# Performance work log

Measured on AMD Instinct MI355X. Metric: run time of the kernel, lower is better.

## Reference

```python
import jax, jax.numpy as jnp
import numpy as np

N_WAY = 5
K_SHOT = 5
TEMPERATURE = 2.0
EPS = 1e-8


def setup_inputs() -> dict:
    key = jax.random.key(0)
    k1, k2, k3, k4 = jax.random.split(key, 4)
    b, q, c, h, w = 4, 75, 640, 10, 10
    support_xf = jax.random.normal(k1, (b, N_WAY * K_SHOT, c, h, w), jnp.float32)
    query_xf = jax.random.normal(k2, (b, q, c, h, w), jnp.float32)
    support_y = jax.random.randint(k3, (b, N_WAY * K_SHOT), 0, N_WAY)
    query_y = jax.random.randint(k4, (b, q), 0, N_WAY)
    return {"support_xf": support_xf, "support_y": support_y,
            "query_xf": query_xf, "query_y": query_y}


def reference(support_xf, support_y, query_xf, query_y):
    b, q, c, h, w = query_xf.shape
    M_q = h * w
    M_s = K_SHOT * h * w  # larger_shot == 'average' -> concat shot descriptors

    # support: [b, n_way*k_shot, c, h, w] -> [b, n_way, c, k_shot*h*w]
    sup = support_xf.reshape(b, N_WAY, K_SHOT, c, h * w)
    sup = jnp.transpose(sup, (0, 1, 3, 2, 4)).reshape(b, N_WAY, c, M_s)
    qf = query_xf.reshape(b, q, c, M_q)

    # cosine similarity over channel dim
    sn = sup / (jnp.linalg.norm(sup, axis=2, keepdims=True) + EPS)
    qn = qf / (jnp.linalg.norm(qf, axis=2, keepdims=True) + EPS)
    # S: [b, q, n_way, M_q, M_s]
    S = jnp.einsum('bqcm,bwcn->bqwmn', qn, sn)

    S_max = S.max(-1)  # [b, q, n_way, M_q]

    # nearest support descriptor (classes merged) for each query descriptor
    S_merged = jnp.transpose(S, (0, 1, 3, 2, 4)).reshape(b, q, M_q, N_WAY * M_s)
    query_nearest = jnp.argmax(S_merged, axis=-1)  # [b, q, M_q]

    # top-2 over class dim of per-class max similarity
    top2 = jax.lax.top_k(jnp.moveaxis(S_max, 2, -1), 2)[0]  # [b, q, M_q, 2]
    query_class_diff = top2[..., 0] - top2[..., 1]  # [b, q, M_q]

    # scatter diffs to the chosen support slot, take max over query positions
    diffs_m = jax.nn.one_hot(query_nearest, N_WAY * M_s, dtype=jnp.float32) \
        * query_class_diff[..., None]  # [b, q, M_q, n_way*M_s]
    diffs_max_nearest = jnp.argmax(diffs_m, axis=-2)  # [b, q, n_way*M_s]

    # mutual-nearest mask: query m is kept iff it is the best query for its slot
    sel = jnp.take_along_axis(diffs_max_nearest, query_nearest, axis=-1)  # [b,q,M_q]
    diff_mask = (sel == jnp.arange(M_q)).astype(jnp.float32) * TEMPERATURE

    predict = (S_max * diff_mask[:, :, None, :]).sum(-1).reshape(b * q, N_WAY)

    logp = jax.nn.log_softmax(predict, axis=-1)
    loss = -jnp.mean(jnp.take_along_axis(logp, query_y.reshape(-1, 1), axis=1))
    return loss
```

## Files before the change

kernel.cpp:

```cpp
#include <hip/hip_runtime.h>
#include <math.h>

#define BB 4
#define QQ 75
#define CC 640
#define HW 100
#define NWAY 5
#define KSHOT 5
#define MS 500
#define MSP 512
#define MTOT 7500
#define MPAD 7680
#define TEMPER 2.0f
#define EPSN 1e-8f
#define LB 32768
#define NCH 8

typedef _Float16 v8h __attribute__((ext_vector_type(8)));
typedef float v4f __attribute__((ext_vector_type(4)));

__device__ inline void splitv(const float* x, v8h& hi, v8h& lo) {
#pragma unroll
    for (int j = 0; j < 8; ++j) {
        _Float16 h = (_Float16)x[j];
        float r0 = x[j] - (float)h;
        hi[j] = h; lo[j] = (_Float16)r0;
    }
}

typedef __attribute__((address_space(3))) unsigned int lds_uint;
typedef __attribute__((address_space(1))) const unsigned int glb_uint;
__device__ inline void gl_lds16(const void* g, void* l) {
    __builtin_amdgcn_global_load_lds((glb_uint*)g, (lds_uint*)l, 16, 0, 0);
}

__global__ __launch_bounds__(128) void norms(const float* __restrict__ qx,
                                             const float* __restrict__ sup,
                                             float* __restrict__ invq,
                                             float* __restrict__ invs,
                                             float* __restrict__ out) {
    int bid = blockIdx.x, t = threadIdx.x;
    if (bid == 0 && t == 0) out[0] = 0.f;
    const float* src; float* dst;
    if (bid < BB * QQ) { src = qx + (size_t)bid * CC * HW; dst = invq + bid * HW; }
    else { int bs = bid - BB * QQ; src = sup + (size_t)bs * CC * HW; dst = invs + bs * HW; }
    if (t < HW) {
        float ss = 0.f;
        for (int c = 0; c < CC; ++c) { float v = src[c * HW + t]; ss += v * v; }
        dst[t] = 1.f / (sqrtf(ss) + EPSN);
    }
}

__global__ __launch_bounds__(256) void prep_AB(const float* __restrict__ qx,
                                               const float* __restrict__ sup,
                                               const float* __restrict__ invs,
                                               _Float16* __restrict__ Ahi,
                                               _Float16* __restrict__ Alo,
                                               _Float16* __restrict__ Bhi,
                                               _Float16* __restrict__ Blo) {
    int g = blockIdx.x;
    const float* src; const float* inv = 0;
    _Float16 *dh, *dl;
    int ct;
    if (g < BB * QQ * 10) {
        int bq = g / 10; ct = g % 10;
        int b = bq / QQ, qi = bq % QQ;
        src = qx + ((size_t)bq * CC + ct * 64) * HW;
        size_t rowbase = (size_t)b * MPAD + qi * HW;
        dh = Ahi + rowbase * CC; dl = Alo + rowbase * CC;
    } else {
        int h = g - BB * QQ * 10;
        int bs = h / 10; ct = h % 10;
        int b = bs / 25, s = bs % 25, w = s / KSHOT, shot = s % KSHOT;
        src = sup + ((size_t)bs * CC + ct * 64) * HW;
        size_t rowbase = (size_t)(b * NWAY + w) * MSP + shot * HW;
        dh = Bhi + rowbase * CC; dl = Blo + rowbase * CC;
        inv = invs + bs * HW;
    }
    __shared__ float tile[64 * 101];
    __shared__ float invt[HW];
    int t = threadIdx.x;
    if (t < HW) invt[t] = inv ? inv[t] : 1.f;
    for (int i = t; i < 64 * HW; i += 256) tile[(i / HW) * 101 + (i % HW)] = src[i];
    __syncthreads();
    for (int cell = t; cell < 800; cell += 256) {
        int p = cell >> 3, oct = cell & 7;
        float iv = invt[p];
        float x[8];
#pragma unroll
        for (int j = 0; j < 8; ++j) x[j] = tile[(oct * 8 + j) * 101 + p] * iv;
        v8h hi, lo; splitv(x, hi, lo);
        size_t off = (size_t)p * CC + ct * 64 + oct * 8;
        *(v8h*)(dh + off) = hi;
        *(v8h*)(dl + off) = lo;
    }
}

__global__ __launch_bounds__(256, 2) void simkernel(
        const _Float16* __restrict__ Ahi, const _Float16* __restrict__ Alo,
        const _Float16* __restrict__ Bhi, const _Float16* __restrict__ Blo,
        float* __restrict__ pmax, unsigned short* __restrict__ pidx) {
    __shared__ char lds_raw[2 * LB];

    int bid = blockIdx.x;
    int mt = bid % 60; int t2 = bid / 60;
    int nt = t2 % 20;  int b = t2 / 20;
    int m0 = mt * 128;
    int w = nt >> 2, n0w = (nt & 3) * 128;

    int tid = threadIdx.x;
    int lane = tid & 63;
    int wvu = __builtin_amdgcn_readfirstlane(tid >> 6);

    const char* abase[4];
    abase[0] = (const char*)(Ahi + ((size_t)b * MPAD + m0) * CC);
    abase[1] = (const char*)(Alo + ((size_t)b * MPAD + m0) * CC);
    abase[2] = (const char*)(Bhi + ((size_t)(b * NWAY + w) * MSP + n0w) * CC);
    abase[3] = (const char*)(Blo + ((size_t)(b * NWAY + w) * MSP + n0w) * CC);

    int rr0 = lane >> 2;
    int oct = (lane & 3) ^ ((lane >> 3) & 3);
    int laneoff = rr0 * (CC * 2) + oct * 16;

    const char* segsrc[8];
    int segoff[8];
#pragma unroll
    for (int s = 0; s < 8; ++s) {
        int g = wvu * 8 + s;
        segsrc[s] = abase[g >> 3] + (size_t)((g & 7) * 16) * (CC * 2) + laneoff;
        segoff[s] = g * 1024;
    }

    int wv = tid >> 6;
    int mrow_w = (wv >> 1) * 64;
    int ncol_w = (wv & 1) * 64;
    int lq = lane >> 4, lc = lane & 15;

    int idxA[4], idxB[4];
#pragma unroll
    for (int mf = 0; mf < 4; ++mf) {
        int row = mrow_w + mf * 16 + lc;
        idxA[mf] = row * 4 + (lq ^ ((row >> 1) & 3));
    }
#pragma unroll
    for (int nf = 0; nf < 4; ++nf) {
        int row = ncol_w + nf * 16 + lc;
        idxB[nf] = row * 4 + (lq ^ ((row >> 1) & 3));
    }

    v4f acc[4][4];
#pragma unroll
    for (int mf = 0; mf < 4; ++mf)
#pragma unroll
        for (int nf = 0; nf < 4; ++nf) acc[mf][nf] = (v4f)0.f;

#pragma unroll
    for (int s = 0; s < 8; ++s)
        gl_lds16(segsrc[s], lds_raw + segoff[s]);

    for (int ch = 0; ch < 20; ++ch) {
        __syncthreads();
        if (ch < 19) {
            int choff = (ch + 1) * 64;
            int dbase = ((ch + 1) & 1) * LB;
#pragma unroll
            for (int s = 0; s < 8; ++s)
                gl_lds16(segsrc[s] + choff, lds_raw + dbase + segoff[s]);
        }
        char* cbuf = lds_raw + (ch & 1) * LB;
        v8h* AHI = (v8h*)cbuf;
        v8h* ALO = (v8h*)(cbuf + 8192);
        v8h* BHI = (v8h*)(cbuf + 16384);
        v8h* BLO = (v8h*)(cbuf + 24576);

        v8h ahi[4], alo[4];
#pragma unroll
        for (int mf = 0; mf < 4; ++mf) { ahi[mf] = AHI[idxA[mf]]; alo[mf] = ALO[idxA[mf]]; }
#pragma unroll
        for (int nf = 0; nf < 4; ++nf) {
            v8h bhi = BHI[idxB[nf]], blo = BLO[idxB[nf]];
#pragma unroll
            for (int mf = 0; mf < 4; ++mf) {
                acc[mf][nf] = __builtin_amdgcn_mfma_f32_16x16x32_f16(ahi[mf], bhi, acc[mf][nf], 0, 0, 0);
                acc[mf][nf] = __builtin_amdgcn_mfma_f32_16x16x32_f16(ahi[mf], blo, acc[mf][nf], 0, 0, 0);
                acc[mf][nf] = __builtin_amdgcn_mfma_f32_16x16x32_f16(alo[mf], bhi, acc[mf][nf], 0, 0, 0);
            }
        }
    }

    int chunk = (nt & 3) * 2 + (wv & 1);
#pragma unroll
    for (int mf = 0; mf < 4; ++mf) {
#pragma unroll
        for (int r = 0; r < 4; ++r) {
            float v = -__builtin_inff(); int idx = 0x7fffffff;
#pragma unroll
            for (int nf = 0; nf < 4; ++nf) {
                int n_way = n0w + ncol_w + nf * 16 + lc;
                float cv = acc[mf][nf][r];
                if (n_way < MS && cv > v) { v = cv; idx = n_way; }
            }
#pragma unroll
            for (int msk = 1; msk < 16; msk <<= 1) {
                float ov = __shfl_xor(v, msk);
                int oi = __shfl_xor(idx, msk);
                if (ov > v || (ov == v && oi < idx)) { v = ov; idx = oi; }
            }
            if (lc == 0) {
                int mrow = m0 + mrow_w + mf * 16 + lq * 4 + r;
                size_t o = ((size_t)(b * NWAY + w) * NCH + chunk) * MPAD + mrow;
                pmax[o] = v;
                pidx[o] = (unsigned short)(idx & 0xffff);
            }
        }
    }
}

__global__ void norm_support(const float* __restrict__ sup, float* __restrict__ snre) {
    int bid = blockIdx.x;
    int b = bid / 25, s = bid % 25;
    int w = s / KSHOT, shot = s % KSHOT;
    const float* src = sup + (size_t)bid * CC * HW;
    float* dst = snre + ((size_t)(b * NWAY + w)) * CC * MSP + shot * HW;
    __shared__ float inv[HW];
    int t = threadIdx.x;
    if (t < HW) {
        float ss = 0.f;
        for (int c = 0; c < CC; ++c) { float v = src[c * HW + t]; ss += v * v; }
        inv[t] = 1.f / (sqrtf(ss) + EPSN);
    }
    __syncthreads();
    for (int i = t; i < CC * HW; i += 256) {
        int c = i / HW, p = i % HW;
        dst[c * MSP + p] = src[i] * inv[p];
    }
    if (shot == KSHOT - 1) {
        float* padbase = snre + ((size_t)(b * NWAY + w)) * CC * MSP;
        for (int i = t; i < CC * (MSP - MS); i += 256) {
            int c = i / (MSP - MS), j = i % (MSP - MS);
            padbase[c * MSP + MS + j] = 0.f;
        }
    }
}

__global__ __launch_bounds__(256) void simkernel_fb(
        const float* __restrict__ qx, const float* __restrict__ snre,
        float* __restrict__ pmax, unsigned short* __restrict__ pidx) {
    __shared__ char lds_fb[49152];
    v8h* AHI = (v8h*)(lds_fb);
    v8h* ALO = (v8h*)(lds_fb + 8192);
    v8h* BHI = (v8h*)(lds_fb + 16384);
    v8h* BLO = (v8h*)(lds_fb + 32768);

    int bid = blockIdx.x;
    int mt = bid % 60; int t2 = bid / 60;
    int nt = t2 % 10;  int b = t2 / 10;
    int m0 = mt * 128;
    int w = nt >> 1;
    int n0w = (nt & 1) * 256;

    int tid = threadIdx.x;
    const float* Abase = qx + (size_t)b * QQ * CC * HW;
    const float* Bbase = snre + (size_t)(b * NWAY + w) * CC * MSP;

    int oct = tid & 3;
    int arow = tid >> 2;
    int aqi[2], ap[2];
#pragma unroll
    for (int pass = 0; pass < 2; ++pass) {
        int mg = m0 + arow + pass * 64;
        if (mg >= MTOT) mg = 0;
        aqi[pass] = mg / HW; ap[pass] = mg % HW;
    }

    v4f acc[4][8];
#pragma unroll
    for (int mf = 0; mf < 4; ++mf)
#pragma unroll
        for (int nf = 0; nf < 8; ++nf) acc[mf][nf] = (v4f)0.f;

    int lane = tid & 63;
    int wv = tid >> 6;
    int mrow_w = (wv >> 1) * 64;
    int ncol_w = (wv & 1) * 128;
    int lq = lane >> 4, lc = lane & 15;

    for (int ch = 0; ch < 20; ++ch) {
        int c0 = ch * 32 + oct * 8;
        __syncthreads();
#pragma unroll
        for (int pass = 0; pass < 2; ++pass) {
            const float* src = Abase + ((size_t)aqi[pass] * CC + c0) * HW + ap[pass];
            float x[8];
#pragma unroll
            for (int j = 0; j < 8; ++j) x[j] = src[j * HW];
            v8h hi, lo; splitv(x, hi, lo);
            int cell = (arow + pass * 64) * 4 + oct;
            AHI[cell] = hi; ALO[cell] = lo;
        }
#pragma unroll
        for (int pass = 0; pass < 4; ++pass) {
            int nrow = arow + pass * 64;
            const float* src = Bbase + (size_t)c0 * MSP + n0w + nrow;
            float x[8];
#pragma unroll
            for (int j = 0; j < 8; ++j) x[j] = src[j * MSP];
            v8h hi, lo; splitv(x, hi, lo);
            int cell = nrow * 4 + oct;
            BHI[cell] = hi; BLO[cell] = lo;
        }
        __syncthreads();

        v8h ahi[4], alo[4];
#pragma unroll
        for (int mf = 0; mf < 4; ++mf) {
            int idx = (mrow_w + mf * 16 + lc) * 4 + lq;
            ahi[mf] = AHI[idx]; alo[mf] = ALO[idx];
        }
#pragma unroll
        for (int nf = 0; nf < 8; ++nf) {
            int idx = (ncol_w + nf * 16 + lc) * 4 + lq;
            v8h bhi = BHI[idx], blo = BLO[idx];
#pragma unroll
            for (int mf = 0; mf < 4; ++mf) {
                acc[mf][nf] = __builtin_amdgcn_mfma_f32_16x16x32_f16(ahi[mf], bhi, acc[mf][nf], 0, 0, 0);
                acc[mf][nf] = __builtin_amdgcn_mfma_f32_16x16x32_f16(ahi[mf], blo, acc[mf][nf], 0, 0, 0);
                acc[mf][nf] = __builtin_amdgcn_mfma_f32_16x16x32_f16(alo[mf], bhi, acc[mf][nf], 0, 0, 0);
            }
        }
    }

    int chunkidx = (nt & 1) * 2 + (wv & 1);
#pragma unroll
    for (int mf = 0; mf < 4; ++mf) {
#pragma unroll
        for (int r = 0; r < 4; ++r) {
            float v = -__builtin_inff(); int idx = 0x7fffffff;
#pragma unroll
            for (int nf = 0; nf < 8; ++nf) {
                int n_way = n0w + ncol_w + nf * 16 + lc;
                float cv = acc[mf][nf][r];
                if (n_way < MS && cv > v) { v = cv; idx = n_way; }
            }
#pragma unroll
            for (int msk = 1; msk < 16; msk <<= 1) {
                float ov = __shfl_xor(v, msk);
                int oi = __shfl_xor(idx, msk);
                if (ov > v || (ov == v && oi < idx)) { v = ov; idx = oi; }
            }
            if (lc == 0) {
                int mrow = m0 + mrow_w + mf * 16 + lq * 4 + r;
                size_t ob = (size_t)(b * NWAY + w) * NCH * MPAD + mrow;
                int s_hi = (idx != 0x7fffffff) ? (idx >> 6) : -1;
#pragma unroll
                for (int sl2 = 0; sl2 < 2; ++sl2) {
                    int sl = chunkidx * 2 + sl2;
                    if (sl == s_hi) {
                        pmax[ob + (size_t)sl * MPAD] = v;
                        pidx[ob + (size_t)sl * MPAD] = (unsigned short)(idx & 0xffff);
                    } else {
                        pmax[ob + (size_t)sl * MPAD] = -__builtin_inff();
                        pidx[ob + (size_t)sl * MPAD] = 0xffffu;
                    }
                }
            }
        }
    }
}

__global__ __launch_bounds__(128) void finalize(
        const float* __restrict__ pmax, const unsigned short* __restrict__ pidx,
        const float* __restrict__ invq, const int* __restrict__ qy,
        float* __restrict__ out) {
    int bq = blockIdx.x;
    int b = bq / QQ, qi = bq % QQ;
    __shared__ float sm[NWAY][HW];
    __shared__ int   si[NWAY][HW];
    __shared__ float diffv[HW];
    __shared__ int   nearest[HW];
    __shared__ float maskv[HW];
    __shared__ float pred[NWAY];
    int t = threadIdx.x;
    if (t < HW) {
        float iq = invq[bq * HW + t];
        for (int w = 0; w < NWAY; ++w) {
            size_t base = ((size_t)(b * NWAY + w) * NCH) * MPAD + qi * HW + t;
            float best = -__builtin_inff(); int bi = 0x7fffffff;
            for (int c = 0; c < NCH; ++c) {
                float v = pmax[base + (size_t)c * MPAD];
                if (v > best) { best = v; bi = pidx[base + (size_t)c * MPAD]; }
            }
            sm[w][t] = best * iq;
            si[w][t] = bi;
        }
    }
    __syncthreads();
    if (t < HW) {
        float v1 = -INFINITY, v2 = -INFINITY;
        float bestv = -INFINITY; int bestslot = 0;
        for (int w = 0; w < NWAY; ++w) {
            float v = sm[w][t];
            if (v > v1) { v2 = v1; v1 = v; } else if (v > v2) { v2 = v; }
            if (v > bestv) { bestv = v; bestslot = w * MS + si[w][t]; }
        }
        diffv[t] = v1 - v2;
        nearest[t] = bestslot;
    }
    __syncthreads();
    if (t < HW) {
        int slot = nearest[t];
        float bv = (nearest[0] == slot) ? diffv[0] : 0.f;
        int bm = 0;
        for (int m = 1; m < HW; ++m) {
            float val = (nearest[m] == slot) ? diffv[m] : 0.f;
            if (val > bv) { bv = val; bm = m; }
        }
        maskv[t] = (bm == t) ? TEMPER : 0.f;
    }
    __syncthreads();
    if (t < NWAY) {
        float s = 0.f;
        for (int m = 0; m < HW; ++m) s += sm[t][m] * maskv[m];
        pred[t] = s;
    }
    __syncthreads();
    if (t == 0) {
        float mx = pred[0];
        for (int w = 1; w < NWAY; ++w) mx = fmaxf(mx, pred[w]);
        float se = 0.f;
        for (int w = 0; w < NWAY; ++w) se += expf(pred[w] - mx);
        float lse = mx + logf(se);
        int y = qy[bq];
        atomicAdd(out, -(pred[y] - lse) * (1.f / (BB * QQ)));
    }
}

extern "C" void kernel_launch(void* const* d_in, const int* in_sizes, int n_in,
                              void* d_out, int out_size, void* d_ws, size_t ws_size,
                              hipStream_t stream) {
    const float* sup = (const float*)d_in[0];
    const float* qx  = (const float*)d_in[2];
    const int*   qy  = (const int*)d_in[3];
    float* out = (float*)d_out;

    size_t pcount = (size_t)BB * NWAY * NCH * MPAD;
    float* pmax = (float*)d_ws;
    unsigned short* pidx = (unsigned short*)(pmax + pcount);
    float* invq = (float*)(pidx + pcount);
    float* invs = invq + (size_t)BB * MTOT;
    char*  big = (char*)(invs + (size_t)BB * 25 * HW);
    size_t header = (size_t)(big - (char*)d_ws);
    size_t needA = (size_t)BB * MPAD * CC * 2;
    size_t needB = (size_t)BB * NWAY * MSP * CC * 2;
    size_t need_fast = header + 2 * (needA + needB);

    hipLaunchKernelGGL(norms, dim3(BB * QQ + BB * 25), dim3(128), 0, stream,
                       qx, sup, invq, invs, out);

    if (ws_size >= need_fast) {
        _Float16* Ahi = (_Float16*)big;
        _Float16* Alo = Ahi + (size_t)BB * MPAD * CC;
        _Float16* Bhi = Alo + (size_t)BB * MPAD * CC;
        _Float16* Blo = Bhi + (size_t)BB * NWAY * MSP * CC;
        hipLaunchKernelGGL(prep_AB, dim3(BB * QQ * 10 + BB * 25 * 10), dim3(256), 0, stream,
                           qx, sup, invs, Ahi, Alo, Bhi, Blo);
        hipLaunchKernelGGL(simkernel, dim3(BB * 20 * 60), dim3(256), 0, stream,
                           Ahi, Alo, Bhi, Blo, pmax, pidx);
    } else {
        float* snre = (float*)big;
        hipLaunchKernelGGL(norm_support, dim3(BB * 25), dim3(256), 0, stream, sup, snre);
        hipLaunchKernelGGL(simkernel_fb, dim3(BB * 10 * 60), dim3(256), 0, stream,
                           qx, snre, pmax, pidx);
    }
    hipLaunchKernelGGL(finalize, dim3(BB * QQ), dim3(128), 0, stream,
                       pmax, pidx, invq, qy, out);
}
```

Measured before the change: 482.7 us.

## Enlarge GEMM tile to 256x256 with 8 waves and staged B triple-buffering

Restructures the split-fp16 similarity GEMM so each block of 512 threads computes a 256x256 tile instead of 128x128, raising operand reuse per LDS load. The A operand stays double-buffered while B moves to a triple-buffered ring loaded one chunk ahead, with manual vmcnt waits and barriers interleaved between MFMA quarters. It also adds s_setprio around MFMA groups. This cuts global/LDS traffic per FLOP but uses 160KB of LDS and more accumulator registers, which lowers occupancy and leaves 1200 blocks for the device.

```diff
diff --git a/kernel.cpp b/kernel.cpp
--- a/kernel.cpp
+++ b/kernel.cpp
@@ -13,8 +13,8 @@
 #define MPAD 7680
 #define TEMPER 2.0f
 #define EPSN 1e-8f
-#define LB 32768
 #define NCH 8
+#define LBS 32768
 
 typedef _Float16 v8h __attribute__((ext_vector_type(8)));
 typedef float v4f __attribute__((ext_vector_type(4)));
@@ -96,107 +96,157 @@
     }
 }
 
-__global__ __launch_bounds__(256, 2) void simkernel(
+__global__ __launch_bounds__(512, 2) void simkernel(
         const _Float16* __restrict__ Ahi, const _Float16* __restrict__ Alo,
         const _Float16* __restrict__ Bhi, const _Float16* __restrict__ Blo,
         float* __restrict__ pmax, unsigned short* __restrict__ pidx) {
-    __shared__ char lds_raw[2 * LB];
+    __shared__ char lds_raw[5 * LBS];
 
     int bid = blockIdx.x;
-    int mt = bid % 60; int t2 = bid / 60;
-    int nt = t2 % 20;  int b = t2 / 20;
-    int m0 = mt * 128;
-    int w = nt >> 2, n0w = (nt & 3) * 128;
+    int nt = bid % 10; int t2 = bid / 10;
+    int mt = t2 % 30;  int b = t2 / 30;
+    int m0 = mt * 256;
+    int w = nt >> 1, n0w = (nt & 1) * 256;
 
     int tid = threadIdx.x;
     int lane = tid & 63;
     int wvu = __builtin_amdgcn_readfirstlane(tid >> 6);
 
-    const char* abase[4];
-    abase[0] = (const char*)(Ahi + ((size_t)b * MPAD + m0) * CC);
-    abase[1] = (const char*)(Alo + ((size_t)b * MPAD + m0) * CC);
-    abase[2] = (const char*)(Bhi + ((size_t)(b * NWAY + w) * MSP + n0w) * CC);
-    abase[3] = (const char*)(Blo + ((size_t)(b * NWAY + w) * MSP + n0w) * CC);
+    int arrA = wvu >> 2;
+    int rgbase = (wvu & 3) * 4;
+    const char* Ab = (const char*)((arrA ? Alo : Ahi) + ((size_t)b * MPAD + m0) * CC);
+    const char* Bb = (const char*)((arrA ? Blo : Bhi) + ((size_t)(b * NWAY + w) * MSP + n0w) * CC);
 
     int rr0 = lane >> 2;
-    int oct = (lane & 3) ^ ((lane >> 3) & 3);
-    int laneoff = rr0 * (CC * 2) + oct * 16;
-
-    const char* segsrc[8];
-    int segoff[8];
-#pragma unroll
-    for (int s = 0; s < 8; ++s) {
-        int g = wvu * 8 + s;
-        segsrc[s] = abase[g >> 3] + (size_t)((g & 7) * 16) * (CC * 2) + laneoff;
-        segoff[s] = g * 1024;
-    }
+    int octsw = (lane & 3) ^ ((lane >> 3) & 3);
+    int laneoff = rr0 * (CC * 2) + octsw * 16;
+
+    const char* srcA[4]; const char* srcB[4]; int dof[4];
+#pragma unroll
+    for (int s = 0; s < 4; ++s) {
+        int rg = rgbase + s;
+        srcA[s] = Ab + (size_t)(rg * 16) * (CC * 2) + laneoff;
+        srcB[s] = Bb + (size_t)(rg * 16) * (CC * 2) + laneoff;
+        dof[s] = arrA * 16384 + rg * 1024;
+    }
+    char* ldsB = lds_raw + 2 * LBS;
 
     int wv = tid >> 6;
-    int mrow_w = (wv >> 1) * 64;
-    int ncol_w = (wv & 1) * 64;
+    int wm = wv >> 2, wn = wv & 3;
     int lq = lane >> 4, lc = lane & 15;
 
     int idxA[4], idxB[4];
 #pragma unroll
     for (int mf = 0; mf < 4; ++mf) {
-        int row = mrow_w + mf * 16 + lc;
+        int row = wm * 128 + mf * 16 + lc;
         idxA[mf] = row * 4 + (lq ^ ((row >> 1) & 3));
     }
 #pragma unroll
     for (int nf = 0; nf < 4; ++nf) {
-        int row = ncol_w + nf * 16 + lc;
+        int row = wn * 64 + nf * 16 + lc;
         idxB[nf] = row * 4 + (lq ^ ((row >> 1) & 3));
     }
 
-    v4f acc[4][4];
-#pragma unroll
-    for (int mf = 0; mf < 4; ++mf)
+    v4f acc[8][4];
+#pragma unroll
+    for (int mf = 0; mf < 8; ++mf)
 #pragma unroll
         for (int nf = 0; nf < 4; ++nf) acc[mf][nf] = (v4f)0.f;
 
 #pragma unroll
-    for (int s = 0; s < 8; ++s)
-        gl_lds16(segsrc[s], lds_raw + segoff[s]);
+    for (int s = 0; s < 4; ++s) gl_lds16(srcA[s], lds_raw + dof[s]);
+#pragma unroll
+    for (int s = 0; s < 4; ++s) gl_lds16(srcB[s], ldsB + dof[s]);
+#pragma unroll
+    for (int s = 0; s < 4; ++s) gl_lds16(srcB[s] + 64, ldsB + LBS + dof[s]);
 
     for (int ch = 0; ch < 20; ++ch) {
-        __syncthreads();
+        if (ch < 19) asm volatile("s_waitcnt vmcnt(4) lgkmcnt(0)\n\ts_barrier" ::: "memory");
+        else         asm volatile("s_waitcnt vmcnt(0) lgkmcnt(0)\n\ts_barrier" ::: "memory");
+
+        const char* cA = lds_raw + (ch & 1) * LBS;
+        const char* cB = ldsB + (ch % 3) * LBS;
+        const v8h* AHI = (const v8h*)cA;
+        const v8h* ALO = (const v8h*)(cA + 16384);
+        const v8h* BHI = (const v8h*)cB;
+        const v8h* BLO = (const v8h*)(cB + 16384);
+        char* nA = lds_raw + ((ch + 1) & 1) * LBS;
+        char* nB = ldsB + ((ch + 2) % 3) * LBS;
+        int offA = (ch + 1) * 64, offB = (ch + 2) * 64;
+
+        v8h ahi[4], alo[4], bhi[4], blo[4];
+
+#pragma unroll
+        for (int m2 = 0; m2 < 4; ++m2) { ahi[m2] = AHI[idxA[m2]]; alo[m2] = ALO[idxA[m2]]; }
+        bhi[0] = BHI[idxB[0]]; blo[0] = BLO[idxB[0]];
+        bhi[1] = BHI[idxB[1]]; blo[1] = BLO[idxB[1]];
         if (ch < 19) {
-            int choff = (ch + 1) * 64;
-            int dbase = ((ch + 1) & 1) * LB;
-#pragma unroll
-            for (int s = 0; s < 8; ++s)
-                gl_lds16(segsrc[s] + choff, lds_raw + dbase + segoff[s]);
-        }
-        char* cbuf = lds_raw + (ch & 1) * LB;
-        v8h* AHI = (v8h*)cbuf;
-        v8h* ALO = (v8h*)(cbuf + 8192);
-        v8h* BHI = (v8h*)(cbuf + 16384);
-        v8h* BLO = (v8h*)(cbuf + 24576);
-
-        v8h ahi[4], alo[4];
-#pragma unroll
-        for (int mf = 0; mf < 4; ++mf) { ahi[mf] = AHI[idxA[mf]]; alo[mf] = ALO[idxA[mf]]; }
-#pragma unroll
-        for (int nf = 0; nf < 4; ++nf) {
-            v8h bhi = BHI[idxB[nf]], blo = BLO[idxB[nf]];
-#pragma unroll
-            for (int mf = 0; mf < 4; ++mf) {
-                acc[mf][nf] = __builtin_amdgcn_mfma_f32_16x16x32_f16(ahi[mf], bhi, acc[mf][nf], 0, 0, 0);
-                acc[mf][nf] = __builtin_amdgcn_mfma_f32_16x16x32_f16(ahi[mf], blo, acc[mf][nf], 0, 0, 0);
-                acc[mf][nf] = __builtin_amdgcn_mfma_f32_16x16x32_f16(alo[mf], bhi, acc[mf][nf], 0, 0, 0);
-            }
-        }
-    }
-
-    int chunk = (nt & 3) * 2 + (wv & 1);
-#pragma unroll
-    for (int mf = 0; mf < 4; ++mf) {
+#pragma unroll
+            for (int s = 0; s < 4; ++s) gl_lds16(srcA[s] + offA, nA + dof[s]);
+        }
+        __builtin_amdgcn_s_setprio(1);
+#pragma unroll
+        for (int n2 = 0; n2 < 2; ++n2)
+#pragma unroll
+            for (int m2 = 0; m2 < 4; ++m2) {
+                acc[m2][n2] = __builtin_amdgcn_mfma_f32_16x16x32_f16(ahi[m2], bhi[n2], acc[m2][n2], 0, 0, 0);
+                acc[m2][n2] = __builtin_amdgcn_mfma_f32_16x16x32_f16(ahi[m2], blo[n2], acc[m2][n2], 0, 0, 0);
+                acc[m2][n2] = __builtin_amdgcn_mfma_f32_16x16x32_f16(alo[m2], bhi[n2], acc[m2][n2], 0, 0, 0);
+            }
+        __builtin_amdgcn_s_setprio(0);
+        __builtin_amdgcn_s_barrier();
+
+        bhi[2] = BHI[idxB[2]]; blo[2] = BLO[idxB[2]];
+        bhi[3] = BHI[idxB[3]]; blo[3] = BLO[idxB[3]];
+        if (ch < 18) { gl_lds16(srcB[0] + offB, nB + dof[0]); gl_lds16(srcB[1] + offB, nB + dof[1]); }
+        __builtin_amdgcn_s_setprio(1);
+#pragma unroll
+        for (int n2 = 2; n2 < 4; ++n2)
+#pragma unroll
+            for (int m2 = 0; m2 < 4; ++m2) {
+                acc[m2][n2] = __builtin_amdgcn_mfma_f32_16x16x32_f16(ahi[m2], bhi[n2], acc[m2][n2], 0, 0, 0);
+                acc[m2][n2] = __builtin_amdgcn_mfma_f32_16x16x32_f16(ahi[m2], blo[n2], acc[m2][n2], 0, 0, 0);
+                acc[m2][n2] = __builtin_amdgcn_mfma_f32_16x16x32_f16(alo[m2], bhi[n2], acc[m2][n2], 0, 0, 0);
+            }
+        __builtin_amdgcn_s_setprio(0);
+        __builtin_amdgcn_s_barrier();
+
+#pragma unroll
+        for (int m2 = 0; m2 < 4; ++m2) { ahi[m2] = AHI[idxA[m2] + 256]; alo[m2] = ALO[idxA[m2] + 256]; }
+        if (ch < 18) { gl_lds16(srcB[2] + offB, nB + dof[2]); gl_lds16(srcB[3] + offB, nB + dof[3]); }
+        __builtin_amdgcn_s_setprio(1);
+#pragma unroll
+        for (int n2 = 0; n2 < 2; ++n2)
+#pragma unroll
+            for (int m2 = 0; m2 < 4; ++m2) {
+                acc[4 + m2][n2] = __builtin_amdgcn_mfma_f32_16x16x32_f16(ahi[m2], bhi[n2], acc[4 + m2][n2], 0, 0, 0);
+                acc[4 + m2][n2] = __builtin_amdgcn_mfma_f32_16x16x32_f16(ahi[m2], blo[n2], acc[4 + m2][n2], 0, 0, 0);
+                acc[4 + m2][n2] = __builtin_amdgcn_mfma_f32_16x16x32_f16(alo[m2], bhi[n2], acc[4 + m2][n2], 0, 0, 0);
+            }
+        __builtin_amdgcn_s_setprio(0);
+        __builtin_amdgcn_s_barrier();
+
+        __builtin_amdgcn_s_setprio(1);
+#pragma unroll
+        for (int n2 = 2; n2 < 4; ++n2)
+#pragma unroll
+            for (int m2 = 0; m2 < 4; ++m2) {
+                acc[4 + m2][n2] = __builtin_amdgcn_mfma_f32_16x16x32_f16(ahi[m2], bhi[n2], acc[4 + m2][n2], 0, 0, 0);
+                acc[4 + m2][n2] = __builtin_amdgcn_mfma_f32_16x16x32_f16(ahi[m2], blo[n2], acc[4 + m2][n2], 0, 0, 0);
+                acc[4 + m2][n2] = __builtin_amdgcn_mfma_f32_16x16x32_f16(alo[m2], bhi[n2], acc[4 + m2][n2], 0, 0, 0);
+            }
+        __builtin_amdgcn_s_setprio(0);
+    }
+
+    int chunk = (nt & 1) * 4 + wn;
+#pragma unroll
+    for (int mf = 0; mf < 8; ++mf) {
 #pragma unroll
         for (int r = 0; r < 4; ++r) {
             float v = -__builtin_inff(); int idx = 0x7fffffff;
 #pragma unroll
             for (int nf = 0; nf < 4; ++nf) {
-                int n_way = n0w + ncol_w + nf * 16 + lc;
+                int n_way = n0w + wn * 64 + nf * 16 + lc;
                 float cv = acc[mf][nf][r];
                 if (n_way < MS && cv > v) { v = cv; idx = n_way; }
             }
@@ -207,7 +257,7 @@
                 if (ov > v || (ov == v && oi < idx)) { v = ov; idx = oi; }
             }
             if (lc == 0) {
-                int mrow = m0 + mrow_w + mf * 16 + lq * 4 + r;
+                int mrow = m0 + wm * 128 + mf * 16 + lq * 4 + r;
                 size_t o = ((size_t)(b * NWAY + w) * NCH + chunk) * MPAD + mrow;
                 pmax[o] = v;
                 pidx[o] = (unsigned short)(idx & 0xffff);
@@ -464,7 +514,7 @@
         _Float16* Blo = Bhi + (size_t)BB * NWAY * MSP * CC;
         hipLaunchKernelGGL(prep_AB, dim3(BB * QQ * 10 + BB * 25 * 10), dim3(256), 0, stream,
                            qx, sup, invs, Ahi, Alo, Bhi, Blo);
-        hipLaunchKernelGGL(simkernel, dim3(BB * 20 * 60), dim3(256), 0, stream,
+        hipLaunchKernelGGL(simkernel, dim3(BB * 30 * 10), dim3(512), 0, stream,
                            Ahi, Alo, Bhi, Blo, pmax, pidx);
     } else {
         float* snre = (float*)big;
```

New measurement: 474.5 us. No clear change (-1.7%).
